# Kernel optimization log

Measured on AMD Instinct MI355X. Metric: run time of the kernel, lower is better.

Reference implementation:

```python
import jax, jax.numpy as jnp
import numpy as np

H = 12          # num attention heads
DH = 64         # head dim
D = H * DH      # hidden size = 768
B, S = 2, 2048


def setup_inputs() -> dict:
    key = jax.random.key(0)
    ks = jax.random.split(key, 8)
    scale = 1.0 / np.sqrt(D)
    return {
        "hidden_states": jax.random.normal(ks[0], (B, S, D), jnp.float32),
        "attention_mask": jnp.zeros((B, 1, 1, S), jnp.float32),
        "position_bias": jax.random.normal(ks[1], (1, H, S, S), jnp.float32) * 0.1,
        "Wq": jax.random.normal(ks[2], (D, D), jnp.float32) * scale,
        "bq": jnp.zeros((D,), jnp.float32),
        "Wk": jax.random.normal(ks[3], (D, D), jnp.float32) * scale,
        "bk": jnp.zeros((D,), jnp.float32),
        "Wv": jax.random.normal(ks[4], (D, D), jnp.float32) * scale,
        "bv": jnp.zeros((D,), jnp.float32),
        "Wo": jax.random.normal(ks[5], (D, D), jnp.float32) * scale,
        "bo": jnp.zeros((D,), jnp.float32),
    }


def reference(hidden_states, attention_mask, position_bias,
              Wq, bq, Wk, bk, Wv, bv, Wo, bo):
    b, s, d = hidden_states.shape
    # Linear projections, then split heads: [B, S, D] -> [B, H, S, DH]
    def split_heads(x):
        return x.reshape(b, s, H, DH).transpose(0, 2, 1, 3)

    q = split_heads(hidden_states @ Wq.T + bq)
    k = split_heads(hidden_states @ Wk.T + bk)
    v = split_heads(hidden_states @ Wv.T + bv)

    # scores: [B, H, S, S]
    scores = jnp.einsum('bhqd,bhkd->bhqk', q, k) / jnp.sqrt(jnp.float32(DH))
    scores = scores + position_bias + attention_mask
    probs = jax.nn.softmax(scores, axis=-1)
    # dropout prob = 0.0 -> identity

    c = jnp.einsum('bhqk,bhkd->bhqd', probs, v)       # [B, H, S, DH]
    c = c.transpose(0, 2, 1, 3).reshape(b, s, d)      # [B, S, D]
    o = c @ Wo.T + bo
    return o
```

## Files before the change

### kernel.cpp

```cpp
#include <hip/hip_runtime.h>

typedef _Float16 f16x8 __attribute__((ext_vector_type(8)));
typedef float f32x4 __attribute__((ext_vector_type(4)));

#define NH 12
#define SEQ 2048
#define DM 768
#define DH 64
#define NROWS 49152

__global__ __launch_bounds__(256) void cast_kernel(
    const float* __restrict__ X, const float* __restrict__ Wq,
    const float* __restrict__ Wk, const float* __restrict__ Wv,
    const float* __restrict__ Wo, _Float16* __restrict__ Xh,
    _Float16* __restrict__ Wall)
{
    size_t base = ((size_t)blockIdx.x * 256 + threadIdx.x) * 8;
    const size_t NX = 3145728, NW = 589824, TOT = NX + 4 * NW;
    if (base >= TOT) return;
    const float* src;
    _Float16* dst;
    if (base < NX) { src = X + base; dst = Xh + base; }
    else {
        size_t r = base - NX;
        int w = (int)(r / NW);
        size_t o = r - (size_t)w * NW;
        src = (w == 0 ? Wq : w == 1 ? Wk : w == 2 ? Wv : Wo) + o;
        dst = Wall + r;
    }
    float4 a = *reinterpret_cast<const float4*>(src);
    float4 b = *reinterpret_cast<const float4*>(src + 4);
    f16x8 h;
    h[0] = (_Float16)a.x; h[1] = (_Float16)a.y; h[2] = (_Float16)a.z; h[3] = (_Float16)a.w;
    h[4] = (_Float16)b.x; h[5] = (_Float16)b.y; h[6] = (_Float16)b.z; h[7] = (_Float16)b.w;
    *reinterpret_cast<f16x8*>(dst) = h;
}

__global__ __launch_bounds__(256) void gemm_kernel(
    const _Float16* __restrict__ A,
    const _Float16* __restrict__ Wbase,
    const float* __restrict__ b0, const float* __restrict__ b1,
    const float* __restrict__ b2,
    _Float16* __restrict__ outQKV, float* __restrict__ outF32, int is_out)
{
    __shared__ _Float16 Asm[128 * 64];
    __shared__ _Float16 Bsm[128 * 64];
    const int tid = threadIdx.x;
    const int m0 = blockIdx.x * 128, n0 = blockIdx.y * 128, z = blockIdx.z;
    const _Float16* Wp = Wbase + (size_t)z * 589824;
    const float* bias = (z == 0) ? b0 : (z == 1 ? b1 : b2);
    const int w = tid >> 6, lane = tid & 63, lr = lane & 15, lg = lane >> 4;
    const int wm = w >> 1, wn = w & 1;

    f32x4 acc[4][4] = {};
    for (int kt = 0; kt < 12; ++kt) {
        __syncthreads();
        #pragma unroll
        for (int i = 0; i < 4; ++i) {
            int c = tid + i * 256;
            int row = c >> 3, col = (c & 7) * 8;
            int sw = (row & 7) << 4;
            f16x8 av = *reinterpret_cast<const f16x8*>(A + (size_t)(m0 + row) * 768 + kt * 64 + col);
            *reinterpret_cast<f16x8*>((char*)Asm + ((row * 128 + col * 2) ^ sw)) = av;
            f16x8 bv = *reinterpret_cast<const f16x8*>(Wp + (size_t)(n0 + row) * 768 + kt * 64 + col);
            *reinterpret_cast<f16x8*>((char*)Bsm + ((row * 128 + col * 2) ^ sw)) = bv;
        }
        __syncthreads();
        #pragma unroll
        for (int kf = 0; kf < 2; ++kf) {
            f16x8 af[4], bf[4];
            #pragma unroll
            for (int mi = 0; mi < 4; ++mi) {
                int row = wm * 64 + mi * 16 + lr;
                af[mi] = *reinterpret_cast<const f16x8*>(
                    (char*)Asm + ((row * 128 + kf * 64 + lg * 16) ^ ((row & 7) << 4)));
            }
            #pragma unroll
            for (int nj = 0; nj < 4; ++nj) {
                int row = wn * 64 + nj * 16 + lr;
                bf[nj] = *reinterpret_cast<const f16x8*>(
                    (char*)Bsm + ((row * 128 + kf * 64 + lg * 16) ^ ((row & 7) << 4)));
            }
            #pragma unroll
            for (int mi = 0; mi < 4; ++mi)
                #pragma unroll
                for (int nj = 0; nj < 4; ++nj)
                    acc[mi][nj] = __builtin_amdgcn_mfma_f32_16x16x32_f16(
                        af[mi], bf[nj], acc[mi][nj], 0, 0, 0);
        }
    }
    #pragma unroll
    for (int mi = 0; mi < 4; ++mi) {
        #pragma unroll
        for (int nj = 0; nj < 4; ++nj) {
            #pragma unroll
            for (int r = 0; r < 4; ++r) {
                int gm = m0 + wm * 64 + mi * 16 + lg * 4 + r;
                int gn = n0 + wn * 64 + nj * 16 + lr;
                float v = acc[mi][nj][r] + bias[gn];
                if (!is_out) {
                    int bb = gm >> 11, s = gm & 2047, hh = gn >> 6, dd = gn & 63;
                    outQKV[(size_t)z * 3145728 +
                           ((((size_t)bb * NH + hh) * SEQ + s) * DH + dd)] = (_Float16)v;
                } else {
                    outF32[(size_t)gm * 768 + gn] = v;
                }
            }
        }
    }
}

__global__ __launch_bounds__(256) void attn_kernel(
    const _Float16* __restrict__ Qh, const _Float16* __restrict__ Kh,
    const _Float16* __restrict__ Vh, const float* __restrict__ pb,
    const float* __restrict__ mask, _Float16* __restrict__ Opart,
    float* __restrict__ ml)
{
    __shared__ _Float16 Kl[64 * 64];
    __shared__ _Float16 Vt[64 * 64];
    __shared__ _Float16 Pl[4 * 16 * 64];
    const int tid = threadIdx.x, w = tid >> 6, lane = tid & 63;
    const int lr = lane & 15, lg = lane >> 4;
    const int lin = blockIdx.x;
    const int xcd = lin & 7, idx = lin >> 3;
    const int bh = xcd * 3 + (idx >> 6);
    const int rem = idx & 63;
    const int q0 = (rem >> 1) << 6;
    const int ks = rem & 1;
    const int kbase = ks << 10;
    const int kend = kbase + 1024;
    const int h = bh % NH, b = bh / NH;
    const size_t headoff = ((size_t)b * NH + h) * SEQ * DH;
    const _Float16* Qp = Qh + headoff;
    const _Float16* Kp = Kh + headoff;
    const _Float16* Vp = Vh + headoff;
    const float L2E = 1.44269504f;

    f16x8 qf[2];
    #pragma unroll
    for (int kf = 0; kf < 2; ++kf)
        qf[kf] = *reinterpret_cast<const f16x8*>(
            Qp + (size_t)(q0 + w * 16 + lr) * DH + kf * 32 + lg * 8);

    const float* pbr[4];
    #pragma unroll
    for (int r = 0; r < 4; ++r)
        pbr[r] = pb + (size_t)h * SEQ * SEQ + (size_t)(q0 + w * 16 + lg * 4 + r) * SEQ;
    const float* mrow = mask + (size_t)b * SEQ;

    f32x4 oacc[4] = {};
    float m_r[4], l_r[4];
    #pragma unroll
    for (int r = 0; r < 4; ++r) { m_r[r] = -3.0e38f; l_r[r] = 0.f; }
    char* Pw = (char*)Pl + w * 2048;

    const int c0 = tid, c1 = tid + 256;
    const int row0 = c0 >> 3, col0 = (c0 & 7) << 3;
    const int row1 = c1 >> 3, col1 = (c1 & 7) << 3;
    f16x8 kn[2], vn[2];

    kn[0] = *reinterpret_cast<const f16x8*>(Kp + (size_t)kbase * DH + c0 * 8);
    kn[1] = *reinterpret_cast<const f16x8*>(Kp + (size_t)kbase * DH + c1 * 8);
    vn[0] = *reinterpret_cast<const f16x8*>(Vp + (size_t)kbase * DH + c0 * 8);
    vn[1] = *reinterpret_cast<const f16x8*>(Vp + (size_t)kbase * DH + c1 * 8);
    float pbc[4][4];
    #pragma unroll
    for (int cf = 0; cf < 4; ++cf) {
        float mk = mrow[kbase + cf * 16 + lr];
        #pragma unroll
        for (int r = 0; r < 4; ++r)
            pbc[cf][r] = (pbr[r][kbase + cf * 16 + lr] + mk) * L2E;
    }
    #pragma unroll
    for (int i = 0; i < 2; ++i) {
        int row = i ? row1 : row0, col = i ? col1 : col0;
        *reinterpret_cast<f16x8*>(
            (char*)Kl + ((row * 128 + col * 2) ^ ((row & 7) << 4))) = kn[i];
        #pragma unroll
        for (int j = 0; j < 8; ++j) {
            int d = col + j;
            *reinterpret_cast<_Float16*>(
                (char*)Vt + ((d * 128 + row * 2) ^ ((((d & 7) ^ ((d >> 3) & 7))) << 4))) = vn[i][j];
        }
    }
    __syncthreads();

    for (int kt0 = kbase; kt0 < kend; kt0 += 64) {
        const int nt = (kt0 + 64 < kend) ? kt0 + 64 : kt0;
        kn[0] = *reinterpret_cast<const f16x8*>(Kp + (size_t)nt * DH + c0 * 8);
        kn[1] = *reinterpret_cast<const f16x8*>(Kp + (size_t)nt * DH + c1 * 8);
        vn[0] = *reinterpret_cast<const f16x8*>(Vp + (size_t)nt * DH + c0 * 8);
        vn[1] = *reinterpret_cast<const f16x8*>(Vp + (size_t)nt * DH + c1 * 8);
        float pbn[4][4];
        #pragma unroll
        for (int cf = 0; cf < 4; ++cf) {
            float mk = mrow[nt + cf * 16 + lr];
            #pragma unroll
            for (int r = 0; r < 4; ++r)
                pbn[cf][r] = (pbr[r][nt + cf * 16 + lr] + mk) * L2E;
        }

        f32x4 sc4[4] = {};
        #pragma unroll
        for (int cf = 0; cf < 4; ++cf) {
            #pragma unroll
            for (int kf = 0; kf < 2; ++kf) {
                f16x8 kb = *reinterpret_cast<const f16x8*>(
                    (char*)Kl + (((cf * 16 + lr) * 128 + kf * 64 + lg * 16) ^ ((lr & 7) << 4)));
                sc4[cf] = __builtin_amdgcn_mfma_f32_16x16x32_f16(qf[kf], kb, sc4[cf], 0, 0, 0);
            }
        }
        float sv[4][4];
        #pragma unroll
        for (int cf = 0; cf < 4; ++cf)
            #pragma unroll
            for (int r = 0; r < 4; ++r)
                sv[cf][r] = sc4[cf][r] * 0.18033688f + pbc[cf][r];

        float rs[4], scale[4];
        #pragma unroll
        for (int r = 0; r < 4; ++r) {
            float t = fmaxf(fmaxf(sv[0][r], sv[1][r]), fmaxf(sv[2][r], sv[3][r]));
            #pragma unroll
            for (int msk = 1; msk < 16; msk <<= 1) t = fmaxf(t, __shfl_xor(t, msk));
            float mn = fmaxf(m_r[r], t);
            scale[r] = exp2f(m_r[r] - mn);
            m_r[r] = mn;
            rs[r] = 0.f;
        }
        #pragma unroll
        for (int cf = 0; cf < 4; ++cf)
            #pragma unroll
            for (int r = 0; r < 4; ++r) {
                float p = exp2f(sv[cf][r] - m_r[r]);
                rs[r] += p;
                int prow = lg * 4 + r;
                *reinterpret_cast<_Float16*>(
                    Pw + ((prow * 128 + (cf * 16 + lr) * 2) ^ ((prow & 7) << 4))) = (_Float16)p;
            }
        #pragma unroll
        for (int r = 0; r < 4; ++r) {
            #pragma unroll
            for (int msk = 1; msk < 16; msk <<= 1) rs[r] += __shfl_xor(rs[r], msk);
            l_r[r] = l_r[r] * scale[r] + rs[r];
        }
        #pragma unroll
        for (int cf = 0; cf < 4; ++cf)
            #pragma unroll
            for (int r = 0; r < 4; ++r) oacc[cf][r] *= scale[r];

        #pragma unroll
        for (int kf = 0; kf < 2; ++kf) {
            f16x8 pa = *reinterpret_cast<const f16x8*>(
                Pw + ((lr * 128 + kf * 64 + lg * 16) ^ ((lr & 7) << 4)));
            #pragma unroll
            for (int cf = 0; cf < 4; ++cf) {
                int d = cf * 16 + lr;
                f16x8 vb = *reinterpret_cast<const f16x8*>(
                    (char*)Vt + ((d * 128 + kf * 64 + lg * 16) ^ ((((d & 7) ^ ((d >> 3) & 7))) << 4)));
                oacc[cf] = __builtin_amdgcn_mfma_f32_16x16x32_f16(pa, vb, oacc[cf], 0, 0, 0);
            }
        }

        __syncthreads();
        #pragma unroll
        for (int i = 0; i < 2; ++i) {
            int row = i ? row1 : row0, col = i ? col1 : col0;
            *reinterpret_cast<f16x8*>(
                (char*)Kl + ((row * 128 + col * 2) ^ ((row & 7) << 4))) = kn[i];
            #pragma unroll
            for (int j = 0; j < 8; ++j) {
                int d = col + j;
                *reinterpret_cast<_Float16*>(
                    (char*)Vt + ((d * 128 + row * 2) ^ ((((d & 7) ^ ((d >> 3) & 7))) << 4))) = vn[i][j];
            }
        }
        #pragma unroll
        for (int cf = 0; cf < 4; ++cf)
            #pragma unroll
            for (int r = 0; r < 4; ++r) pbc[cf][r] = pbn[cf][r];
        __syncthreads();
    }

    #pragma unroll
    for (int r = 0; r < 4; ++r) {
        int grow = q0 + w * 16 + lg * 4 + r;
        size_t rowi = ((size_t)b * NH + h) * SEQ + grow;
        _Float16* od = Opart + ((size_t)ks * NROWS + rowi) * DH;
        #pragma unroll
        for (int cf = 0; cf < 4; ++cf)
            od[cf * 16 + lr] = (_Float16)oacc[cf][r];
        if (lr == 0) {
            ml[rowi * 4 + ks * 2 + 0] = m_r[r];
            ml[rowi * 4 + ks * 2 + 1] = l_r[r];
        }
    }
}

__global__ __launch_bounds__(256) void merge_kernel(
    const _Float16* __restrict__ Opart, const float* __restrict__ ml,
    _Float16* __restrict__ ctx)
{
    int gid = blockIdx.x * 256 + threadIdx.x;
    int row = gid >> 3, d8 = (gid & 7) << 3;
    const size_t NP = (size_t)NROWS * DH;
    f16x8 o0 = *reinterpret_cast<const f16x8*>(Opart + (size_t)row * DH + d8);
    f16x8 o1 = *reinterpret_cast<const f16x8*>(Opart + NP + (size_t)row * DH + d8);
    float4 m = *reinterpret_cast<const float4*>(ml + (size_t)row * 4);
    float M = fmaxf(m.x, m.z);
    float a0 = exp2f(m.x - M), a1 = exp2f(m.z - M);
    float inv = 1.0f / (a0 * m.y + a1 * m.w);
    a0 *= inv; a1 *= inv;
    f16x8 o;
    #pragma unroll
    for (int j = 0; j < 8; ++j)
        o[j] = (_Float16)(a0 * (float)o0[j] + a1 * (float)o1[j]);
    int b = row / (NH * SEQ);
    int hs = row - b * (NH * SEQ);
    int h = hs >> 11, s = hs & 2047;
    *reinterpret_cast<f16x8*>(ctx + ((size_t)b * SEQ + s) * DM + h * DH + d8) = o;
}

extern "C" void kernel_launch(void* const* d_in, const int* in_sizes, int n_in,
                              void* d_out, int out_size, void* d_ws, size_t ws_size,
                              hipStream_t stream) {
    const float* X    = (const float*)d_in[0];
    const float* mask = (const float*)d_in[1];
    const float* pb   = (const float*)d_in[2];
    const float* Wq   = (const float*)d_in[3];
    const float* bq   = (const float*)d_in[4];
    const float* Wk   = (const float*)d_in[5];
    const float* bk   = (const float*)d_in[6];
    const float* Wv   = (const float*)d_in[7];
    const float* bv   = (const float*)d_in[8];
    const float* Wo   = (const float*)d_in[9];
    const float* bo   = (const float*)d_in[10];
    float* out = (float*)d_out;

    _Float16* Xh    = (_Float16*)d_ws;
    _Float16* Wall  = Xh + 3145728;
    _Float16* QKV   = Wall + 4 * 589824;
    _Float16* ctx   = QKV + 3 * 3145728;
    _Float16* Opart = ctx + 3145728;
    float*    ml    = (float*)(Opart + 2 * 3145728);

    cast_kernel<<<2688, 256, 0, stream>>>(X, Wq, Wk, Wv, Wo, Xh, Wall);
    gemm_kernel<<<dim3(32, 6, 3), 256, 0, stream>>>(
        Xh, Wall, bq, bk, bv, QKV, nullptr, 0);
    attn_kernel<<<1536, 256, 0, stream>>>(
        QKV, QKV + 3145728, QKV + 2 * 3145728, pb, mask, Opart, ml);
    merge_kernel<<<1536, 256, 0, stream>>>(Opart, ml, ctx);
    gemm_kernel<<<dim3(32, 6, 1), 256, 0, stream>>>(
        ctx, Wall + 3 * 589824, bo, bo, bo, nullptr, out, 1);
}
```

Baseline: 190.2 us.

## Emit V transposed from projection GEMM and double query rows per attention block

The QKV projection GEMM now writes V in head-dim-major (transposed) layout, so the attention kernel can load V tiles with vector stores instead of scattered per-element transposes into shared memory. Each attention wave now handles 32 query rows instead of 16, reusing each K/V shared-memory fragment across two MFMA tiles, and the block count is halved. The score MFMA operands are swapped so position-bias loads become float4 reads along the key axis. This raises register pressure (launch bounds min 3 blocks) and enlarges the P buffer, and the transposed V writes from the GEMM epilogue are strided.

```diff
diff --git a/kernel.cpp b/kernel.cpp
--- a/kernel.cpp
+++ b/kernel.cpp
@@ -1,6 +1,7 @@
 #include <hip/hip_runtime.h>
 
 typedef _Float16 f16x8 __attribute__((ext_vector_type(8)));
+typedef _Float16 f16x4 __attribute__((ext_vector_type(4)));
 typedef float f32x4 __attribute__((ext_vector_type(4)));
 
 #define NH 12
@@ -41,7 +42,8 @@
     const _Float16* __restrict__ Wbase,
     const float* __restrict__ b0, const float* __restrict__ b1,
     const float* __restrict__ b2,
-    _Float16* __restrict__ outQKV, float* __restrict__ outF32, int is_out)
+    _Float16* __restrict__ outQKV, _Float16* __restrict__ outVT,
+    float* __restrict__ outF32, int is_out)
 {
     __shared__ _Float16 Asm[128 * 64];
     __shared__ _Float16 Bsm[128 * 64];
@@ -100,8 +102,11 @@
                 float v = acc[mi][nj][r] + bias[gn];
                 if (!is_out) {
                     int bb = gm >> 11, s = gm & 2047, hh = gn >> 6, dd = gn & 63;
-                    outQKV[(size_t)z * 3145728 +
-                           ((((size_t)bb * NH + hh) * SEQ + s) * DH + dd)] = (_Float16)v;
+                    if (z == 2)
+                        outVT[(((size_t)bb * NH + hh) * DH + dd) * SEQ + s] = (_Float16)v;
+                    else
+                        outQKV[(size_t)z * 3145728 +
+                               ((((size_t)bb * NH + hh) * SEQ + s) * DH + dd)] = (_Float16)v;
                 } else {
                     outF32[(size_t)gm * 768 + gn] = v;
                 }
@@ -110,189 +115,184 @@
     }
 }
 
-__global__ __launch_bounds__(256) void attn_kernel(
+__global__ __launch_bounds__(256, 3) void attn_kernel(
     const _Float16* __restrict__ Qh, const _Float16* __restrict__ Kh,
-    const _Float16* __restrict__ Vh, const float* __restrict__ pb,
+    const _Float16* __restrict__ VTg, const float* __restrict__ pb,
     const float* __restrict__ mask, _Float16* __restrict__ Opart,
     float* __restrict__ ml)
 {
     __shared__ _Float16 Kl[64 * 64];
     __shared__ _Float16 Vt[64 * 64];
-    __shared__ _Float16 Pl[4 * 16 * 64];
+    __shared__ _Float16 Pl[4 * 32 * 64];
     const int tid = threadIdx.x, w = tid >> 6, lane = tid & 63;
     const int lr = lane & 15, lg = lane >> 4;
     const int lin = blockIdx.x;
     const int xcd = lin & 7, idx = lin >> 3;
-    const int bh = xcd * 3 + (idx >> 6);
-    const int rem = idx & 63;
-    const int q0 = (rem >> 1) << 6;
+    const int bh = xcd * 3 + idx / 32;
+    const int rem = idx & 31;
+    const int q0 = (rem >> 1) << 7;
     const int ks = rem & 1;
-    const int kbase = ks << 10;
-    const int kend = kbase + 1024;
+    const int kbase = ks << 10, kend = kbase + 1024;
     const int h = bh % NH, b = bh / NH;
-    const size_t headoff = ((size_t)b * NH + h) * SEQ * DH;
+    const size_t headoff = (size_t)bh * SEQ * DH;
     const _Float16* Qp = Qh + headoff;
     const _Float16* Kp = Kh + headoff;
-    const _Float16* Vp = Vh + headoff;
+    const _Float16* VTp = VTg + headoff;
     const float L2E = 1.44269504f;
 
-    f16x8 qf[2];
-    #pragma unroll
-    for (int kf = 0; kf < 2; ++kf)
-        qf[kf] = *reinterpret_cast<const f16x8*>(
-            Qp + (size_t)(q0 + w * 16 + lr) * DH + kf * 32 + lg * 8);
-
-    const float* pbr[4];
-    #pragma unroll
-    for (int r = 0; r < 4; ++r)
-        pbr[r] = pb + (size_t)h * SEQ * SEQ + (size_t)(q0 + w * 16 + lg * 4 + r) * SEQ;
+    f16x8 qfr[2][2];
+    #pragma unroll
+    for (int qf = 0; qf < 2; ++qf)
+        #pragma unroll
+        for (int kf = 0; kf < 2; ++kf)
+            qfr[qf][kf] = *reinterpret_cast<const f16x8*>(
+                Qp + (size_t)(q0 + w * 32 + qf * 16 + lr) * DH + kf * 32 + lg * 8);
+
+    const float* pbq[2];
+    #pragma unroll
+    for (int qf = 0; qf < 2; ++qf)
+        pbq[qf] = pb + (size_t)h * SEQ * SEQ + (size_t)(q0 + w * 32 + qf * 16 + lr) * SEQ;
     const float* mrow = mask + (size_t)b * SEQ;
 
-    f32x4 oacc[4] = {};
-    float m_r[4], l_r[4];
-    #pragma unroll
-    for (int r = 0; r < 4; ++r) { m_r[r] = -3.0e38f; l_r[r] = 0.f; }
-    char* Pw = (char*)Pl + w * 2048;
+    f32x4 oacc[2][4] = {};
+    float m_r[2] = {-3.0e38f, -3.0e38f}, l_r[2] = {0.f, 0.f};
+    char* Pw = (char*)Pl + w * 4096;
+    char* KlB = (char*)Kl;
+    char* VtB = (char*)Vt;
 
     const int c0 = tid, c1 = tid + 256;
     const int row0 = c0 >> 3, col0 = (c0 & 7) << 3;
     const int row1 = c1 >> 3, col1 = (c1 & 7) << 3;
     f16x8 kn[2], vn[2];
 
-    kn[0] = *reinterpret_cast<const f16x8*>(Kp + (size_t)kbase * DH + c0 * 8);
-    kn[1] = *reinterpret_cast<const f16x8*>(Kp + (size_t)kbase * DH + c1 * 8);
-    vn[0] = *reinterpret_cast<const f16x8*>(Vp + (size_t)kbase * DH + c0 * 8);
-    vn[1] = *reinterpret_cast<const f16x8*>(Vp + (size_t)kbase * DH + c1 * 8);
-    float pbc[4][4];
+    kn[0] = *reinterpret_cast<const f16x8*>(Kp + (size_t)(kbase + row0) * DH + col0);
+    kn[1] = *reinterpret_cast<const f16x8*>(Kp + (size_t)(kbase + row1) * DH + col1);
+    vn[0] = *reinterpret_cast<const f16x8*>(VTp + (size_t)row0 * SEQ + kbase + col0);
+    vn[1] = *reinterpret_cast<const f16x8*>(VTp + (size_t)row1 * SEQ + kbase + col1);
+    f32x4 pbc[2][4];
     #pragma unroll
     for (int cf = 0; cf < 4; ++cf) {
-        float mk = mrow[kbase + cf * 16 + lr];
-        #pragma unroll
-        for (int r = 0; r < 4; ++r)
-            pbc[cf][r] = (pbr[r][kbase + cf * 16 + lr] + mk) * L2E;
-    }
-    #pragma unroll
-    for (int i = 0; i < 2; ++i) {
-        int row = i ? row1 : row0, col = i ? col1 : col0;
-        *reinterpret_cast<f16x8*>(
-            (char*)Kl + ((row * 128 + col * 2) ^ ((row & 7) << 4))) = kn[i];
-        #pragma unroll
-        for (int j = 0; j < 8; ++j) {
-            int d = col + j;
-            *reinterpret_cast<_Float16*>(
-                (char*)Vt + ((d * 128 + row * 2) ^ ((((d & 7) ^ ((d >> 3) & 7))) << 4))) = vn[i][j];
-        }
-    }
+        f32x4 mk = *reinterpret_cast<const f32x4*>(mrow + kbase + cf * 16 + lg * 4);
+        #pragma unroll
+        for (int qf = 0; qf < 2; ++qf)
+            pbc[qf][cf] = (*reinterpret_cast<const f32x4*>(pbq[qf] + kbase + cf * 16 + lg * 4) + mk) * L2E;
+    }
+    *reinterpret_cast<f16x8*>(KlB + ((row0 * 128 + col0 * 2) ^ ((row0 & 7) << 4))) = kn[0];
+    *reinterpret_cast<f16x8*>(KlB + ((row1 * 128 + col1 * 2) ^ ((row1 & 7) << 4))) = kn[1];
+    *reinterpret_cast<f16x8*>(VtB + ((row0 * 128 + col0 * 2) ^ ((row0 & 7) << 4))) = vn[0];
+    *reinterpret_cast<f16x8*>(VtB + ((row1 * 128 + col1 * 2) ^ ((row1 & 7) << 4))) = vn[1];
     __syncthreads();
 
     for (int kt0 = kbase; kt0 < kend; kt0 += 64) {
         const int nt = (kt0 + 64 < kend) ? kt0 + 64 : kt0;
-        kn[0] = *reinterpret_cast<const f16x8*>(Kp + (size_t)nt * DH + c0 * 8);
-        kn[1] = *reinterpret_cast<const f16x8*>(Kp + (size_t)nt * DH + c1 * 8);
-        vn[0] = *reinterpret_cast<const f16x8*>(Vp + (size_t)nt * DH + c0 * 8);
-        vn[1] = *reinterpret_cast<const f16x8*>(Vp + (size_t)nt * DH + c1 * 8);
-        float pbn[4][4];
+        kn[0] = *reinterpret_cast<const f16x8*>(Kp + (size_t)(nt + row0) * DH + col0);
+        kn[1] = *reinterpret_cast<const f16x8*>(Kp + (size_t)(nt + row1) * DH + col1);
+        vn[0] = *reinterpret_cast<const f16x8*>(VTp + (size_t)row0 * SEQ + nt + col0);
+        vn[1] = *reinterpret_cast<const f16x8*>(VTp + (size_t)row1 * SEQ + nt + col1);
+
+        f32x4 sc[2][4] = {};
         #pragma unroll
         for (int cf = 0; cf < 4; ++cf) {
-            float mk = mrow[nt + cf * 16 + lr];
-            #pragma unroll
-            for (int r = 0; r < 4; ++r)
-                pbn[cf][r] = (pbr[r][nt + cf * 16 + lr] + mk) * L2E;
-        }
-
-        f32x4 sc4[4] = {};
+            #pragma unroll
+            for (int kf = 0; kf < 2; ++kf) {
+                f16x8 ka = *reinterpret_cast<const f16x8*>(
+                    KlB + (((cf * 16 + lr) * 128 + kf * 64 + lg * 16) ^ ((lr & 7) << 4)));
+                #pragma unroll
+                for (int qf = 0; qf < 2; ++qf)
+                    sc[qf][cf] = __builtin_amdgcn_mfma_f32_16x16x32_f16(
+                        ka, qfr[qf][kf], sc[qf][cf], 0, 0, 0);
+            }
+        }
+        #pragma unroll
+        for (int qf = 0; qf < 2; ++qf)
+            #pragma unroll
+            for (int cf = 0; cf < 4; ++cf)
+                sc[qf][cf] = sc[qf][cf] * 0.18033688f + pbc[qf][cf];
+
         #pragma unroll
         for (int cf = 0; cf < 4; ++cf) {
-            #pragma unroll
-            for (int kf = 0; kf < 2; ++kf) {
-                f16x8 kb = *reinterpret_cast<const f16x8*>(
-                    (char*)Kl + (((cf * 16 + lr) * 128 + kf * 64 + lg * 16) ^ ((lr & 7) << 4)));
-                sc4[cf] = __builtin_amdgcn_mfma_f32_16x16x32_f16(qf[kf], kb, sc4[cf], 0, 0, 0);
-            }
-        }
-        float sv[4][4];
-        #pragma unroll
-        for (int cf = 0; cf < 4; ++cf)
-            #pragma unroll
-            for (int r = 0; r < 4; ++r)
-                sv[cf][r] = sc4[cf][r] * 0.18033688f + pbc[cf][r];
-
-        float rs[4], scale[4];
+            f32x4 mk = *reinterpret_cast<const f32x4*>(mrow + nt + cf * 16 + lg * 4);
+            #pragma unroll
+            for (int qf = 0; qf < 2; ++qf)
+                pbc[qf][cf] = (*reinterpret_cast<const f32x4*>(pbq[qf] + nt + cf * 16 + lg * 4) + mk) * L2E;
+        }
+
+        #pragma unroll
+        for (int qf = 0; qf < 2; ++qf) {
+            float t = sc[qf][0][0];
+            #pragma unroll
+            for (int cf = 0; cf < 4; ++cf)
+                #pragma unroll
+                for (int r = 0; r < 4; ++r) t = fmaxf(t, sc[qf][cf][r]);
+            t = fmaxf(t, __shfl_xor(t, 16));
+            t = fmaxf(t, __shfl_xor(t, 32));
+            float mn = fmaxf(m_r[qf], t);
+            float srow = exp2f(m_r[qf] - mn);
+            m_r[qf] = mn;
+            float rs = 0.f;
+            const int qrow = qf * 16 + lr;
+            #pragma unroll
+            for (int cf = 0; cf < 4; ++cf) {
+                f16x4 pv;
+                #pragma unroll
+                for (int r = 0; r < 4; ++r) {
+                    float p = exp2f(sc[qf][cf][r] - mn);
+                    rs += p;
+                    pv[r] = (_Float16)p;
+                }
+                *reinterpret_cast<f16x4*>(
+                    Pw + ((qrow * 128 + cf * 32 + lg * 8) ^ ((lr & 7) << 4))) = pv;
+            }
+            rs += __shfl_xor(rs, 16);
+            rs += __shfl_xor(rs, 32);
+            l_r[qf] = l_r[qf] * srow + rs;
+            float s0 = __shfl(srow, lg * 4 + 0);
+            float s1 = __shfl(srow, lg * 4 + 1);
+            float s2 = __shfl(srow, lg * 4 + 2);
+            float s3 = __shfl(srow, lg * 4 + 3);
+            f32x4 scv = {s0, s1, s2, s3};
+            #pragma unroll
+            for (int cf = 0; cf < 4; ++cf) oacc[qf][cf] *= scv;
+        }
+
+        #pragma unroll
+        for (int kf = 0; kf < 2; ++kf) {
+            f16x8 pa0 = *reinterpret_cast<const f16x8*>(
+                Pw + ((lr * 128 + kf * 64 + lg * 16) ^ ((lr & 7) << 4)));
+            f16x8 pa1 = *reinterpret_cast<const f16x8*>(
+                Pw + (((16 + lr) * 128 + kf * 64 + lg * 16) ^ ((lr & 7) << 4)));
+            #pragma unroll
+            for (int cf = 0; cf < 4; ++cf) {
+                f16x8 vb = *reinterpret_cast<const f16x8*>(
+                    VtB + (((cf * 16 + lr) * 128 + kf * 64 + lg * 16) ^ ((lr & 7) << 4)));
+                oacc[0][cf] = __builtin_amdgcn_mfma_f32_16x16x32_f16(pa0, vb, oacc[0][cf], 0, 0, 0);
+                oacc[1][cf] = __builtin_amdgcn_mfma_f32_16x16x32_f16(pa1, vb, oacc[1][cf], 0, 0, 0);
+            }
+        }
+
+        __syncthreads();
+        *reinterpret_cast<f16x8*>(KlB + ((row0 * 128 + col0 * 2) ^ ((row0 & 7) << 4))) = kn[0];
+        *reinterpret_cast<f16x8*>(KlB + ((row1 * 128 + col1 * 2) ^ ((row1 & 7) << 4))) = kn[1];
+        *reinterpret_cast<f16x8*>(VtB + ((row0 * 128 + col0 * 2) ^ ((row0 & 7) << 4))) = vn[0];
+        *reinterpret_cast<f16x8*>(VtB + ((row1 * 128 + col1 * 2) ^ ((row1 & 7) << 4))) = vn[1];
+        __syncthreads();
+    }
+
+    #pragma unroll
+    for (int qf = 0; qf < 2; ++qf) {
+        size_t rowbase = (size_t)bh * SEQ + q0 + w * 32 + qf * 16;
+        if (lane < 16) {
+            size_t rowi = rowbase + lr;
+            ml[rowi * 4 + ks * 2 + 0] = m_r[qf];
+            ml[rowi * 4 + ks * 2 + 1] = l_r[qf];
+        }
         #pragma unroll
         for (int r = 0; r < 4; ++r) {
-            float t = fmaxf(fmaxf(sv[0][r], sv[1][r]), fmaxf(sv[2][r], sv[3][r]));
-            #pragma unroll
-            for (int msk = 1; msk < 16; msk <<= 1) t = fmaxf(t, __shfl_xor(t, msk));
-            float mn = fmaxf(m_r[r], t);
-            scale[r] = exp2f(m_r[r] - mn);
-            m_r[r] = mn;
-            rs[r] = 0.f;
-        }
-        #pragma unroll
-        for (int cf = 0; cf < 4; ++cf)
-            #pragma unroll
-            for (int r = 0; r < 4; ++r) {
-                float p = exp2f(sv[cf][r] - m_r[r]);
-                rs[r] += p;
-                int prow = lg * 4 + r;
-                *reinterpret_cast<_Float16*>(
-                    Pw + ((prow * 128 + (cf * 16 + lr) * 2) ^ ((prow & 7) << 4))) = (_Float16)p;
-            }
-        #pragma unroll
-        for (int r = 0; r < 4; ++r) {
-            #pragma unroll
-            for (int msk = 1; msk < 16; msk <<= 1) rs[r] += __shfl_xor(rs[r], msk);
-            l_r[r] = l_r[r] * scale[r] + rs[r];
-        }
-        #pragma unroll
-        for (int cf = 0; cf < 4; ++cf)
-            #pragma unroll
-            for (int r = 0; r < 4; ++r) oacc[cf][r] *= scale[r];
-
-        #pragma unroll
-        for (int kf = 0; kf < 2; ++kf) {
-            f16x8 pa = *reinterpret_cast<const f16x8*>(
-                Pw + ((lr * 128 + kf * 64 + lg * 16) ^ ((lr & 7) << 4)));
-            #pragma unroll
-            for (int cf = 0; cf < 4; ++cf) {
-                int d = cf * 16 + lr;
-                f16x8 vb = *reinterpret_cast<const f16x8*>(
-                    (char*)Vt + ((d * 128 + kf * 64 + lg * 16) ^ ((((d & 7) ^ ((d >> 3) & 7))) << 4)));
-                oacc[cf] = __builtin_amdgcn_mfma_f32_16x16x32_f16(pa, vb, oacc[cf], 0, 0, 0);
-            }
-        }
-
-        __syncthreads();
-        #pragma unroll
-        for (int i = 0; i < 2; ++i) {
-            int row = i ? row1 : row0, col = i ? col1 : col0;
-            *reinterpret_cast<f16x8*>(
-                (char*)Kl + ((row * 128 + col * 2) ^ ((row & 7) << 4))) = kn[i];
-            #pragma unroll
-            for (int j = 0; j < 8; ++j) {
-                int d = col + j;
-                *reinterpret_cast<_Float16*>(
-                    (char*)Vt + ((d * 128 + row * 2) ^ ((((d & 7) ^ ((d >> 3) & 7))) << 4))) = vn[i][j];
-            }
-        }
-        #pragma unroll
-        for (int cf = 0; cf < 4; ++cf)
-            #pragma unroll
-            for (int r = 0; r < 4; ++r) pbc[cf][r] = pbn[cf][r];
-        __syncthreads();
-    }
-
-    #pragma unroll
-    for (int r = 0; r < 4; ++r) {
-        int grow = q0 + w * 16 + lg * 4 + r;
-        size_t rowi = ((size_t)b * NH + h) * SEQ + grow;
-        _Float16* od = Opart + ((size_t)ks * NROWS + rowi) * DH;
-        #pragma unroll
-        for (int cf = 0; cf < 4; ++cf)
-            od[cf * 16 + lr] = (_Float16)oacc[cf][r];
-        if (lr == 0) {
-            ml[rowi * 4 + ks * 2 + 0] = m_r[r];
-            ml[rowi * 4 + ks * 2 + 1] = l_r[r];
+            size_t rowi = rowbase + lg * 4 + r;
+            _Float16* od = Opart + ((size_t)ks * NROWS + rowi) * DH;
+            #pragma unroll
+            for (int cf = 0; cf < 4; ++cf)
+                od[cf * 16 + lr] = (_Float16)oacc[qf][cf][r];
         }
     }
 }
@@ -339,17 +339,18 @@
 
     _Float16* Xh    = (_Float16*)d_ws;
     _Float16* Wall  = Xh + 3145728;
-    _Float16* QKV   = Wall + 4 * 589824;
-    _Float16* ctx   = QKV + 3 * 3145728;
+    _Float16* QK    = Wall + 4 * 589824;
+    _Float16* VT    = QK + 2 * 3145728;
+    _Float16* ctx   = VT + 3145728;
     _Float16* Opart = ctx + 3145728;
     float*    ml    = (float*)(Opart + 2 * 3145728);
 
     cast_kernel<<<2688, 256, 0, stream>>>(X, Wq, Wk, Wv, Wo, Xh, Wall);
     gemm_kernel<<<dim3(32, 6, 3), 256, 0, stream>>>(
-        Xh, Wall, bq, bk, bv, QKV, nullptr, 0);
-    attn_kernel<<<1536, 256, 0, stream>>>(
-        QKV, QKV + 3145728, QKV + 2 * 3145728, pb, mask, Opart, ml);
+        Xh, Wall, bq, bk, bv, QK, VT, nullptr, 0);
+    attn_kernel<<<768, 256, 0, stream>>>(
+        QK, QK + 3145728, VT, pb, mask, Opart, ml);
     merge_kernel<<<1536, 256, 0, stream>>>(Opart, ml, ctx);
     gemm_kernel<<<dim3(32, 6, 1), 256, 0, stream>>>(
-        ctx, Wall + 3 * 589824, bo, bo, bo, nullptr, out, 1);
-}
+        ctx, Wall + 3 * 589824, bo, bo, bo, nullptr, nullptr, out, 1);
+}
```

Measured after the change: 192.3 us. No clear change (+1.1%).
